# Kernel tuning notes

Measured on AMD Instinct MI355X. Metric: run time of the kernel, lower is better.

## Reference

```python
import jax, jax.numpy as jnp
import numpy as np

NUM_HEADS = 16
HEAD_DIM = 64
HIDDEN = NUM_HEADS * HEAD_DIM  # 1024
BATCH, SEQ = 4, 2048


def setup_inputs() -> dict:
    key = jax.random.key(0)
    k1, k2, k3, k4 = jax.random.split(key, 4)
    hidden_states = jax.random.normal(k1, (BATCH, SEQ, HIDDEN), dtype=jnp.float32)
    attention_mask = jnp.arange(SEQ)[None, :] < int(SEQ * 0.9)
    attention_mask = jnp.broadcast_to(attention_mask, (BATCH, SEQ))
    s_in = 1.0 / np.sqrt(HIDDEN)
    Wqkv = jax.random.normal(k2, (HIDDEN, 3 * HIDDEN), dtype=jnp.float32) * s_in
    Wout = jax.random.normal(k3, (HIDDEN, HIDDEN), dtype=jnp.float32) * s_in
    bout = jnp.zeros((HIDDEN,), dtype=jnp.float32)
    return {"hidden_states": hidden_states, "attention_mask": attention_mask,
            "Wqkv": Wqkv, "Wout": Wout, "bout": bout}


def reference(hidden_states, attention_mask, Wqkv, Wout, bout):
    B, S, H = hidden_states.shape
    qkv = hidden_states @ Wqkv  # [B,S,3*H]
    qkv = qkv.reshape(B, S, 3, NUM_HEADS, HEAD_DIM)
    qkv = jnp.transpose(qkv, (2, 0, 3, 1, 4))  # [3,B,nh,S,hd]
    q, k, v = qkv[0], qkv[1], qkv[2]
    scale = 1.0 / jnp.sqrt(jnp.float32(HEAD_DIM))
    attn = jnp.einsum('bhid,bhjd->bhij', q, k) * scale  # [B,nh,S,S]
    bias = jnp.where(attention_mask[:, None, None, :], 0.0,
                     jnp.finfo(jnp.float32).min)
    attn = attn + bias
    attn = jax.nn.softmax(attn, axis=-1)
    out = jnp.einsum('bhij,bhjd->bhid', attn, v)  # [B,nh,S,hd]
    out = jnp.transpose(out, (0, 2, 1, 3)).reshape(B, S, H)
    return out @ Wout + bout
```

## Files before the change

kernel.cpp:

```cpp
#include <hip/hip_runtime.h>


typedef short bh8 __attribute__((ext_vector_type(8)));
typedef short bh4 __attribute__((ext_vector_type(4)));
typedef float f32x4 __attribute__((ext_vector_type(4)));

#define B_ 4
#define S_ 2048
#define NH_ 16
#define HD_ 64
#define H_ 1024

__device__ inline short f2bf(float f) {
    unsigned u = __builtin_bit_cast(unsigned, f);
    u = (u + 0x7fffu + ((u >> 16) & 1u)) >> 16;
    return (short)u;
}

__device__ inline unsigned pk2bf(float a, float b) {
#if __has_builtin(__builtin_amdgcn_cvt_pk_bf16_f32)
    auto r = __builtin_amdgcn_cvt_pk_bf16_f32(a, b);
    return __builtin_bit_cast(unsigned, r);
#else
    unsigned ua = __builtin_bit_cast(unsigned, a) + 0x8000u;
    unsigned ub = __builtin_bit_cast(unsigned, b) + 0x8000u;
    return __builtin_amdgcn_perm(ub, ua, 0x07060302);
#endif
}

__global__ void cvt_f32_bf16(const float* __restrict__ in, short* __restrict__ out, int n) {
    int i = (blockIdx.x * 256 + threadIdx.x) * 4;
    if (i + 3 < n) {
        float4 v = *(const float4*)(in + i);
        union { short s[4]; unsigned long long u; } r;
        r.s[0] = f2bf(v.x); r.s[1] = f2bf(v.y); r.s[2] = f2bf(v.z); r.s[3] = f2bf(v.w);
        *(unsigned long long*)(out + i) = r.u;
    }
}

__global__ void transpose_cvt(const float* __restrict__ in, short* __restrict__ out,
                              int K, int N, int qcols, float qs) {
    __shared__ float tile[32][33];
    int n0 = blockIdx.x * 32, k0 = blockIdx.y * 32;
    int tx = threadIdx.x, ty = threadIdx.y;
#pragma unroll
    for (int i = 0; i < 32; i += 8)
        tile[ty + i][tx] = in[(long)(k0 + ty + i) * N + n0 + tx];
    __syncthreads();
#pragma unroll
    for (int i = 0; i < 32; i += 8) {
        int n = n0 + ty + i;
        float v = tile[tx][ty + i];
        if (n < qcols) v *= qs;
        out[(long)n * K + k0 + tx] = f2bf(v);
    }
}

__global__ void make_bias(const int* __restrict__ mask, float* __restrict__ biasf, int n) {
    int i = blockIdx.x * 256 + threadIdx.x;
    if (i < n) biasf[i] = mask[i] ? 0.0f : -1e30f;
}

__global__ void make_tilelist(const int* __restrict__ mask, int* __restrict__ tl) {
    int b = blockIdx.x, t = threadIdx.x;
    int flag = 0;
    if (t < 32) {
        bool anyA = false, anyM = false;
        for (int i = 0; i < 64; ++i) {
            int m = mask[b * S_ + t * 64 + i];
            anyA |= (m != 0); anyM |= (m == 0);
        }
        flag = anyA ? (anyM ? 1 : 2) : 0;
    }
    unsigned long long act = __ballot(flag != 0);
    int pos = __popcll(act & ((1ull << t) - 1ull));
    if (flag) tl[b * 33 + 1 + pos] = t | (flag << 16);
    if (t == 0) tl[b * 33] = __popcll(act);
}

__global__ __launch_bounds__(256, 2) void gemm_bf16(
    const short* __restrict__ A, const short* __restrict__ Bt,
    int M, int N, int K, int mode,
    short* __restrict__ qk, short* __restrict__ vt,
    const float* __restrict__ bias, float* __restrict__ out) {
    __shared__ short smem[128 * 136];
    short* sA[2] = { smem, smem + 4096 };
    short* sB[2] = { smem + 8192, smem + 12288 };
    int tid = threadIdx.x;
    int lane = tid & 63, wid = tid >> 6;
    int quad = lane >> 4, l15 = lane & 15;
    int wy = wid >> 1, wx = wid & 1;
    int m0 = blockIdx.y * 128, n0 = blockIdx.x * 128;

    f32x4 acc[4][4] = {};
    const short* Ag = A + (long)m0 * K;
    const short* Bg = Bt + (long)n0 * K;

    for (int k0 = 0; k0 < K; k0 += 64) {
#pragma unroll
        for (int half = 0; half < 2; ++half) {
#pragma unroll
            for (int i = 0; i < 2; ++i) {
                int flat = i * 256 + tid;
                int r = flat >> 2, c = (flat & 3) << 3;
                __builtin_amdgcn_global_load_lds(
                    (const __attribute__((address_space(1))) void*)(Ag + (long)r * K + k0 + half * 32 + c),
                    (__attribute__((address_space(3))) void*)(sA[half] + i * 2048 + wid * 512),
                    16, 0, 0);
                __builtin_amdgcn_global_load_lds(
                    (const __attribute__((address_space(1))) void*)(Bg + (long)r * K + k0 + half * 32 + c),
                    (__attribute__((address_space(3))) void*)(sB[half] + i * 2048 + wid * 512),
                    16, 0, 0);
            }
        }
        __syncthreads();
#pragma unroll
        for (int half = 0; half < 2; ++half) {
            bh8 af[4], bfr[4];
#pragma unroll
            for (int mi = 0; mi < 4; ++mi)
                af[mi] = *(const bh8*)(sA[half] + (wy * 64 + mi * 16 + l15) * 32 + quad * 8);
#pragma unroll
            for (int ni = 0; ni < 4; ++ni)
                bfr[ni] = *(const bh8*)(sB[half] + (wx * 64 + ni * 16 + l15) * 32 + quad * 8);
#pragma unroll
            for (int mi = 0; mi < 4; ++mi)
#pragma unroll
                for (int ni = 0; ni < 4; ++ni)
                    acc[mi][ni] = __builtin_amdgcn_mfma_f32_16x16x32_bf16(af[mi], bfr[ni], acc[mi][ni], 0, 0, 0);
        }
        __syncthreads();
    }

    if (mode == 0) {
        bool isV = (n0 >= 2048);
#pragma unroll
        for (int mi = 0; mi < 4; ++mi)
#pragma unroll
            for (int ni = 0; ni < 4; ++ni) {
                int c = wx * 64 + ni * 16 + l15;
                int rb = wy * 64 + mi * 16 + quad * 4;
#pragma unroll
                for (int reg = 0; reg < 4; ++reg) {
                    short hv = f2bf(acc[mi][ni][reg]);
                    if (isV) smem[c * 136 + rb + reg] = hv;
                    else     smem[(rb + reg) * 136 + c] = hv;
                }
            }
        __syncthreads();
        int b = m0 >> 11, sbase = m0 & 2047;
#pragma unroll
        for (int j = 0; j < 8; ++j) {
            int f = (j * 256 + tid) * 8;
            int i0 = f >> 7, i1 = f & 127;
            bh8 v = *(const bh8*)(smem + i0 * 136 + i1);
            if (isV) {
                int cc = n0 - 2048 + i0;
                int h = cc >> 6, d = cc & 63;
                *(bh8*)(vt + ((long)(b * NH_ + h) * HD_ + d) * S_ + sbase + i1) = v;
            } else {
                *(bh8*)(qk + (long)(m0 + i0) * 2048 + n0 + i1) = v;
            }
        }
    } else {
#pragma unroll
        for (int mi = 0; mi < 4; ++mi)
#pragma unroll
            for (int ni = 0; ni < 4; ++ni) {
                int gc = n0 + wx * 64 + ni * 16 + l15;
                float bv = bias[gc];
#pragma unroll
                for (int reg = 0; reg < 4; ++reg) {
                    int gr = m0 + wy * 64 + mi * 16 + quad * 4 + reg;
                    out[(long)gr * N + gc] = acc[mi][ni][reg] + bv;
                }
            }
    }
}

__device__ inline void ld_tile(const short* __restrict__ Kb, const short* __restrict__ Vb,
                               int j0, int tid, bh8* kp, bh8* vp) {
#pragma unroll
    for (int i = 0; i < 2; ++i) {
        int flat = i * 256 + tid;
        int r = flat >> 3, c = (flat & 7) << 3;
        kp[i] = *(const bh8*)(Kb + (long)(j0 + r) * 2048 + c);
        vp[i] = *(const bh8*)(Vb + (long)r * S_ + j0 + c);
    }
}
__device__ inline void st_tile(short* lk, short* lv, int tid, const bh8* kp, const bh8* vp) {
#pragma unroll
    for (int i = 0; i < 2; ++i) {
        int flat = i * 256 + tid;
        int r = flat >> 3, c = (flat & 7) << 3;
        *(bh8*)(lk + r * 72 + c) = kp[i];
        *(bh8*)(lv + r * 72 + c) = vp[i];
    }
}

__global__ __launch_bounds__(256, 2) void attn_fwd(
    const short* __restrict__ QK, const short* __restrict__ Vtw,
    const float* __restrict__ biasf, const int* __restrict__ tl,
    short* __restrict__ Aout) {
    __shared__ short lK[2][64 * 72];
    __shared__ short lV[2][64 * 72];
    int tid = threadIdx.x;
    int lane = tid & 63, w = tid >> 6;
    int quad = lane >> 4, l15 = lane & 15;
    int p = blockIdx.x;
    int b = p >> 4, h = p & 15;
    int qbase = blockIdx.y * 256 + w * 64;

    const short* Kb = QK + (long)b * S_ * 2048 + 1024 + h * HD_;
    const short* Vb = Vtw + (long)p * HD_ * S_;

    bh8 qf[4][2];
#pragma unroll
    for (int mi = 0; mi < 4; ++mi)
#pragma unroll
        for (int ks = 0; ks < 2; ++ks)
            qf[mi][ks] = *(const bh8*)(QK + (long)(b * S_ + qbase + mi * 16 + l15) * 2048
                                       + h * HD_ + ks * 32 + quad * 8);

    f32x4 o[4][4] = {};
    f32x4 ls[4] = {};
    const bh8 ones = {0x3F80, 0x3F80, 0x3F80, 0x3F80, 0x3F80, 0x3F80, 0x3F80, 0x3F80};

    int cnt = tl[b * 33];
    int e0 = tl[b * 33 + 1];
    int j0 = (e0 & 0xffff) << 6, flag = e0 >> 16;
    bh8 kp[2], vp[2];
    ld_tile(Kb, Vb, j0, tid, kp, vp);
    st_tile(lK[0], lV[0], tid, kp, vp);
    int cur = 0;

    for (int it = 0; it < cnt; ++it) {
        __syncthreads();
        bool more = (it + 1 < cnt);
        int nj0 = 0, nflag = 0;
        if (more) {
            int en = tl[b * 33 + 2 + it];
            nj0 = (en & 0xffff) << 6; nflag = en >> 16;
            ld_tile(Kb, Vb, nj0, tid, kp, vp);
        }
        const short* ck = lK[cur];
        const short* cv = lV[cur];

        bh4 pf[4][4];
#pragma unroll
        for (int nj = 0; nj < 4; ++nj) {
            f32x4 scn[4] = {};
#pragma unroll
            for (int ks = 0; ks < 2; ++ks) {
                bh8 kf = *(const bh8*)(ck + (nj * 16 + l15) * 72 + ks * 32 + quad * 8);
#pragma unroll
                for (int mi = 0; mi < 4; ++mi)
                    scn[mi] = __builtin_amdgcn_mfma_f32_16x16x32_bf16(kf, qf[mi][ks], scn[mi], 0, 0, 0);
            }
            if (flag == 1) {
                f32x4 bb = *(const f32x4*)(biasf + b * S_ + j0 + nj * 16 + quad * 4);
#pragma unroll
                for (int mi = 0; mi < 4; ++mi) {
#pragma unroll
                    for (int r = 0; r < 4; ++r) scn[mi][r] += bb[r];
                }
            }
#pragma unroll
            for (int mi = 0; mi < 4; ++mi) {
                unsigned u0 = pk2bf(__builtin_amdgcn_exp2f(scn[mi][0]),
                                    __builtin_amdgcn_exp2f(scn[mi][1]));
                unsigned u1 = pk2bf(__builtin_amdgcn_exp2f(scn[mi][2]),
                                    __builtin_amdgcn_exp2f(scn[mi][3]));
                uint2 uu = {u0, u1};
                pf[nj][mi] = __builtin_bit_cast(bh4, uu);
            }
        }

#pragma unroll
        for (int pr = 0; pr < 2; ++pr) {
            int njA = 2 * pr, njB = 2 * pr + 1;
            bh8 a[4];
#pragma unroll
            for (int mi = 0; mi < 4; ++mi)
                a[mi] = __builtin_shufflevector(pf[njA][mi], pf[njB][mi], 0, 1, 2, 3, 4, 5, 6, 7);
#pragma unroll
            for (int mi = 0; mi < 4; ++mi)
                ls[mi] = __builtin_amdgcn_mfma_f32_16x16x32_bf16(a[mi], ones, ls[mi], 0, 0, 0);
#pragma unroll
            for (int nd = 0; nd < 4; ++nd) {
                bh4 v0 = *(const bh4*)(cv + (nd * 16 + l15) * 72 + njA * 16 + quad * 4);
                bh4 v1 = *(const bh4*)(cv + (nd * 16 + l15) * 72 + njB * 16 + quad * 4);
                bh8 vf = __builtin_shufflevector(v0, v1, 0, 1, 2, 3, 4, 5, 6, 7);
#pragma unroll
                for (int mi = 0; mi < 4; ++mi)
                    o[mi][nd] = __builtin_amdgcn_mfma_f32_16x16x32_bf16(a[mi], vf, o[mi][nd], 0, 0, 0);
            }
        }

        if (more) st_tile(lK[cur ^ 1], lV[cur ^ 1], tid, kp, vp);
        j0 = nj0; flag = nflag; cur ^= 1;
    }

#pragma unroll
    for (int mi = 0; mi < 4; ++mi)
#pragma unroll
        for (int nd = 0; nd < 4; ++nd)
#pragma unroll
            for (int reg = 0; reg < 4; ++reg) {
                int s = qbase + mi * 16 + quad * 4 + reg;
                int col = h * HD_ + nd * 16 + l15;
                float v = o[mi][nd][reg] / ls[mi][reg];
                Aout[((long)b * S_ + s) * H_ + col] = f2bf(v);
            }
}

extern "C" void kernel_launch(void* const* d_in, const int* in_sizes, int n_in,
                              void* d_out, int out_size, void* d_ws, size_t ws_size,
                              hipStream_t stream) {
    const float* hidden = (const float*)d_in[0];
    const int* mask = (const int*)d_in[1];
    const float* Wqkv = (const float*)d_in[2];
    const float* Wout = (const float*)d_in[3];
    const float* bout = (const float*)d_in[4];
    float* out = (float*)d_out;

    char* ws = (char*)d_ws;
    const size_t XBF = 0;
    const size_t WQKVT = 16777216;
    const size_t WOUTT = WQKVT + 6291456;
    const size_t QKO = WOUTT + 2097152;
    const size_t VT = QKO + 33554432;

    short* Xbf = (short*)(ws + XBF);
    short* WqkvT = (short*)(ws + WQKVT);
    short* WoutT = (short*)(ws + WOUTT);
    short* QK = (short*)(ws + QKO);
    short* Vt = (short*)(ws + VT);
    short* Aout = Xbf;
    float* biasf = (float*)WqkvT;
    int* tl = (int*)(ws + WQKVT + 32768);

    const float Cs = 0.18033688011112042f;

    cvt_f32_bf16<<<dim3(8192), dim3(256), 0, stream>>>(hidden, Xbf, B_ * S_ * H_);
    transpose_cvt<<<dim3(96, 32), dim3(32, 8), 0, stream>>>(Wqkv, WqkvT, H_, 3 * H_, H_, Cs);
    transpose_cvt<<<dim3(32, 32), dim3(32, 8), 0, stream>>>(Wout, WoutT, H_, H_, 0, 1.0f);

    gemm_bf16<<<dim3(24, 64), dim3(256), 0, stream>>>(
        Xbf, WqkvT, B_ * S_, 3 * H_, H_, 0, QK, Vt, nullptr, nullptr);

    make_bias<<<dim3(32), dim3(256), 0, stream>>>(mask, biasf, B_ * S_);
    make_tilelist<<<dim3(4), dim3(64), 0, stream>>>(mask, tl);

    attn_fwd<<<dim3(64, 8), dim3(256), 0, stream>>>(QK, Vt, biasf, tl, Aout);

    gemm_bf16<<<dim3(8, 64), dim3(256), 0, stream>>>(
        Aout, WoutT, B_ * S_, H_, H_, 1, nullptr, nullptr, bout, out);
}
```

Before: 261.7 us.

## Use 512-thread attention blocks sharing K/V tiles and add MFMA priority hints

The attention kernel now launches 512-thread blocks that each cover 512 queries, so each K/V tile staged in LDS is shared by eight waves instead of four. This halves K/V global traffic per query and gives each thread a single 16-byte load per tile. It also raises wave priority around the MFMA bursts with s_setprio, and replaces the per-element division in the epilogue with one reciprocal per row. Risks are a larger register budget under launch_bounds(512,2), fewer blocks in the grid (256), and slightly different rounding from the approximate reciprocal.

After: 263.3 us. No clear change (+0.6%).

```diff
diff --git a/kernel.cpp b/kernel.cpp
--- a/kernel.cpp
+++ b/kernel.cpp
@@ -180,25 +180,17 @@
 
 __device__ inline void ld_tile(const short* __restrict__ Kb, const short* __restrict__ Vb,
                                int j0, int tid, bh8* kp, bh8* vp) {
-#pragma unroll
-    for (int i = 0; i < 2; ++i) {
-        int flat = i * 256 + tid;
-        int r = flat >> 3, c = (flat & 7) << 3;
-        kp[i] = *(const bh8*)(Kb + (long)(j0 + r) * 2048 + c);
-        vp[i] = *(const bh8*)(Vb + (long)r * S_ + j0 + c);
-    }
-}
-__device__ inline void st_tile(short* lk, short* lv, int tid, const bh8* kp, const bh8* vp) {
-#pragma unroll
-    for (int i = 0; i < 2; ++i) {
-        int flat = i * 256 + tid;
-        int r = flat >> 3, c = (flat & 7) << 3;
-        *(bh8*)(lk + r * 72 + c) = kp[i];
-        *(bh8*)(lv + r * 72 + c) = vp[i];
-    }
-}
-
-__global__ __launch_bounds__(256, 2) void attn_fwd(
+    int r = tid >> 3, c = (tid & 7) << 3;
+    *kp = *(const bh8*)(Kb + (long)(j0 + r) * 2048 + c);
+    *vp = *(const bh8*)(Vb + (long)r * S_ + j0 + c);
+}
+__device__ inline void st_tile(short* lk, short* lv, int tid, bh8 kp, bh8 vp) {
+    int r = tid >> 3, c = (tid & 7) << 3;
+    *(bh8*)(lk + r * 72 + c) = kp;
+    *(bh8*)(lv + r * 72 + c) = vp;
+}
+
+__global__ __launch_bounds__(512, 2) void attn_fwd(
     const short* __restrict__ QK, const short* __restrict__ Vtw,
     const float* __restrict__ biasf, const int* __restrict__ tl,
     short* __restrict__ Aout) {
@@ -209,7 +201,7 @@
     int quad = lane >> 4, l15 = lane & 15;
     int p = blockIdx.x;
     int b = p >> 4, h = p & 15;
-    int qbase = blockIdx.y * 256 + w * 64;
+    int qbase = blockIdx.y * 512 + w * 64;
 
     const short* Kb = QK + (long)b * S_ * 2048 + 1024 + h * HD_;
     const short* Vb = Vtw + (long)p * HD_ * S_;
@@ -229,8 +221,8 @@
     int cnt = tl[b * 33];
     int e0 = tl[b * 33 + 1];
     int j0 = (e0 & 0xffff) << 6, flag = e0 >> 16;
-    bh8 kp[2], vp[2];
-    ld_tile(Kb, Vb, j0, tid, kp, vp);
+    bh8 kp, vp;
+    ld_tile(Kb, Vb, j0, tid, &kp, &vp);
     st_tile(lK[0], lV[0], tid, kp, vp);
     int cur = 0;
 
@@ -241,7 +233,7 @@
         if (more) {
             int en = tl[b * 33 + 2 + it];
             nj0 = (en & 0xffff) << 6; nflag = en >> 16;
-            ld_tile(Kb, Vb, nj0, tid, kp, vp);
+            ld_tile(Kb, Vb, nj0, tid, &kp, &vp);
         }
         const short* ck = lK[cur];
         const short* cv = lV[cur];
@@ -250,13 +242,16 @@
 #pragma unroll
         for (int nj = 0; nj < 4; ++nj) {
             f32x4 scn[4] = {};
-#pragma unroll
-            for (int ks = 0; ks < 2; ++ks) {
-                bh8 kf = *(const bh8*)(ck + (nj * 16 + l15) * 72 + ks * 32 + quad * 8);
-#pragma unroll
-                for (int mi = 0; mi < 4; ++mi)
-                    scn[mi] = __builtin_amdgcn_mfma_f32_16x16x32_bf16(kf, qf[mi][ks], scn[mi], 0, 0, 0);
-            }
+            bh8 kf0 = *(const bh8*)(ck + (nj * 16 + l15) * 72 + quad * 8);
+            bh8 kf1 = *(const bh8*)(ck + (nj * 16 + l15) * 72 + 32 + quad * 8);
+            __builtin_amdgcn_s_setprio(1);
+#pragma unroll
+            for (int mi = 0; mi < 4; ++mi)
+                scn[mi] = __builtin_amdgcn_mfma_f32_16x16x32_bf16(kf0, qf[mi][0], scn[mi], 0, 0, 0);
+#pragma unroll
+            for (int mi = 0; mi < 4; ++mi)
+                scn[mi] = __builtin_amdgcn_mfma_f32_16x16x32_bf16(kf1, qf[mi][1], scn[mi], 0, 0, 0);
+            __builtin_amdgcn_s_setprio(0);
             if (flag == 1) {
                 f32x4 bb = *(const f32x4*)(biasf + b * S_ + j0 + nj * 16 + quad * 4);
 #pragma unroll
@@ -283,6 +278,7 @@
 #pragma unroll
             for (int mi = 0; mi < 4; ++mi)
                 a[mi] = __builtin_shufflevector(pf[njA][mi], pf[njB][mi], 0, 1, 2, 3, 4, 5, 6, 7);
+            __builtin_amdgcn_s_setprio(1);
 #pragma unroll
             for (int mi = 0; mi < 4; ++mi)
                 ls[mi] = __builtin_amdgcn_mfma_f32_16x16x32_bf16(a[mi], ones, ls[mi], 0, 0, 0);
@@ -295,6 +291,7 @@
                 for (int mi = 0; mi < 4; ++mi)
                     o[mi][nd] = __builtin_amdgcn_mfma_f32_16x16x32_bf16(a[mi], vf, o[mi][nd], 0, 0, 0);
             }
+            __builtin_amdgcn_s_setprio(0);
         }
 
         if (more) st_tile(lK[cur ^ 1], lV[cur ^ 1], tid, kp, vp);
@@ -304,14 +301,15 @@
 #pragma unroll
     for (int mi = 0; mi < 4; ++mi)
 #pragma unroll
-        for (int nd = 0; nd < 4; ++nd)
-#pragma unroll
-            for (int reg = 0; reg < 4; ++reg) {
-                int s = qbase + mi * 16 + quad * 4 + reg;
+        for (int reg = 0; reg < 4; ++reg) {
+            float inv = __builtin_amdgcn_rcpf(ls[mi][reg]);
+            int s = qbase + mi * 16 + quad * 4 + reg;
+#pragma unroll
+            for (int nd = 0; nd < 4; ++nd) {
                 int col = h * HD_ + nd * 16 + l15;
-                float v = o[mi][nd][reg] / ls[mi][reg];
-                Aout[((long)b * S_ + s) * H_ + col] = f2bf(v);
-            }
+                Aout[((long)b * S_ + s) * H_ + col] = f2bf(o[mi][nd][reg] * inv);
+            }
+        }
 }
 
 extern "C" void kernel_launch(void* const* d_in, const int* in_sizes, int n_in,
@@ -352,7 +350,7 @@
     make_bias<<<dim3(32), dim3(256), 0, stream>>>(mask, biasf, B_ * S_);
     make_tilelist<<<dim3(4), dim3(64), 0, stream>>>(mask, tl);
 
-    attn_fwd<<<dim3(64, 8), dim3(256), 0, stream>>>(QK, Vt, biasf, tl, Aout);
+    attn_fwd<<<dim3(64, 4), dim3(512), 0, stream>>>(QK, Vt, biasf, tl, Aout);
 
     gemm_bf16<<<dim3(8, 64), dim3(256), 0, stream>>>(
         Aout, WoutT, B_ * S_, H_, H_, 1, nullptr, nullptr, bout, out);
```
